# Optimization experiments

Measured on AMD Instinct MI355X. Metric: run time of the kernel, lower is better.

Reference implementation:

```python
import jax, jax.numpy as jnp
import numpy as np

WINDOW_SIZE = 7
C1 = 0.01 ** 2
C2 = 0.03 ** 2


def _gaussian_window(ws: int) -> jnp.ndarray:
    sigma = ws / 6.0
    coords = jnp.arange(ws, dtype=jnp.float32) - ws // 2
    g = jnp.exp(-coords ** 2 / (2 * sigma ** 2))
    g = g / g.sum()
    k3 = g[:, None, None] * g[None, :, None] * g[None, None, :]
    k3 = k3 / k3.sum()
    return k3.reshape(1, 1, ws, ws, ws)  # OIDHW


def _conv3d_same(x, w):
    pad = WINDOW_SIZE // 2
    return jax.lax.conv_general_dilated(
        x, w, window_strides=(1, 1, 1),
        padding=[(pad, pad)] * 3,
        dimension_numbers=('NCDHW', 'OIDHW', 'NCDHW'))


def setup_inputs() -> dict:
    key = jax.random.key(0)
    k1, k2 = jax.random.split(key)
    shape = (2, 1, 160, 160, 160)
    predicted = jax.random.uniform(k1, shape, dtype=jnp.float32)
    target = jax.random.uniform(k2, shape, dtype=jnp.float32)
    return {"predicted": predicted, "target": target}


def reference(predicted, target):
    window = _gaussian_window(WINDOW_SIZE)
    mu1 = _conv3d_same(predicted, window)
    mu2 = _conv3d_same(target, window)
    mu1_sq = mu1 ** 2
    mu2_sq = mu2 ** 2
    mu1_mu2 = mu1 * mu2
    sigma1_sq = _conv3d_same(predicted ** 2, window) - mu1_sq
    sigma2_sq = _conv3d_same(target ** 2, window) - mu2_sq
    sigma12 = _conv3d_same(predicted * target, window) - mu1_mu2
    ssim_map = ((2 * mu1_mu2 + C1) * (2 * sigma12 + C2)) / (
        (mu1_sq + mu2_sq + C1) * (sigma1_sq + sigma2_sq + C2))
    return 1.0 - ssim_map.mean()
```

## Files before the change

kernel.cpp:

```cpp
#include <hip/hip_runtime.h>
#include <math.h>

#define DD 160
#define HH 160
#define WW 160
#define NB 2
#define NEL (NB*DD*HH*WW)

#define XT 32
#define YT 16
#define ZC 16
#define NTHR 256
#define NZCH (DD/ZC)
#define GX (WW/XT)
#define GY (HH/YT)
#define NBLK (GX*GY*NB*NZCH)
#define NPART (NBLK*4)

#define HR 22
#define NJOB (HR*8)
#define CP 35

typedef float v2f __attribute__((ext_vector_type(2)));

struct G7 { float g[7]; };

__global__ __launch_bounds__(NTHR, 4) void ssim_fused(
        const float* __restrict__ p, const float* __restrict__ t,
        float* __restrict__ partial, G7 gw) {
    const int tid = threadIdx.x;
    const int lane = tid & 63, wv = tid >> 6;
    const int tx  = tid & 31;
    const int tyo = tid >> 5;

    const int flat = blockIdx.x;
    const int w = (flat & 7) * (NBLK / 8) + (flat >> 3);
    const int bx = w % GX;
    const int by = (w / GX) % GY;
    const int bz = w / (GX * GY);

    const int x0 = bx * XT;
    const int y0 = by * YT;
    const int n  = bz / NZCH;
    const int zs = (bz % NZCH) * ZC;
    const int send = zs + ZC + 3;

    __shared__ float4 c4[2][HR][CP];

    v2f r01[2][6], r23[2][6];
#pragma unroll
    for (int yo = 0; yo < 2; ++yo)
#pragma unroll
        for (int j = 0; j < 6; ++j) {
            r01[yo][j] = (v2f)(0.f);
            r23[yo][j] = (v2f)(0.f);
        }

    const float C1v = 1e-4f, C2v = 9e-4f;
    float ssum = 0.f;
    const int hw = HH * WW;
    const float* pv = p + (size_t)n * DD * hw;
    const float* tv = t + (size_t)n * DD * hw;

    const int br = tid >> 3;
    const int bxg = tid & 7;
    const int bgy = y0 + br - 3;
    const bool jok = tid < NJOB;
    const bool browok = jok && (unsigned)bgy < (unsigned)HH;
    const int cbase = x0 + 4 * bxg - 4;
    const int pcr = tx + (tx >> 3);
    bool qok[3];
#pragma unroll
    for (int q = 0; q < 3; ++q)
        qok[q] = browok && (unsigned)(cbase + 4 * q) < (unsigned)WW;

    const float* prow = pv + (size_t)(zs - 3) * hw + bgy * WW;
    const float* trow = tv + (size_t)(zs - 3) * hw + bgy * WW;

    float4 pfa[3], pfb[3];
    auto prefetch = [&](int sx) {
#pragma unroll
        for (int q = 0; q < 3; ++q) {
            pfa[q] = make_float4(0.f, 0.f, 0.f, 0.f);
            pfb[q] = make_float4(0.f, 0.f, 0.f, 0.f);
        }
        if (sx >= 0 && sx < DD && sx < send) {
#pragma unroll
            for (int q = 0; q < 3; ++q) {
                if (qok[q]) {
                    pfa[q] = *(const float4*)(prow + cbase + 4 * q);
                    pfb[q] = *(const float4*)(trow + cbase + 4 * q);
                }
            }
        }
    };

    auto do_B = [&](int par) {
        if (jok) {
            v2f s01[4], s23[4];
#pragma unroll
            for (int e = 0; e < 4; ++e) { s01[e] = (v2f)(0.f); s23[e] = (v2f)(0.f); }
#pragma unroll
            for (int q = 0; q < 3; ++q) {
                const float af[4] = {pfa[q].x, pfa[q].y, pfa[q].z, pfa[q].w};
                const float bf[4] = {pfb[q].x, pfb[q].y, pfb[q].z, pfb[q].w};
#pragma unroll
                for (int jj = 0; jj < 4; ++jj) {
                    const int i = 4 * q + jj;
                    v2f pt; pt[0] = af[jj]; pt[1] = bf[jj];
                    v2f ud; ud[0] = af[jj] + bf[jj]; ud[1] = af[jj] - bf[jj];
                    v2f qu = ud * ud;
#pragma unroll
                    for (int e = 0; e < 4; ++e) {
                        const int k = i - e - 1;
                        if (k >= 0 && k < 7) {
                            s01[e] = gw.g[k] * pt + s01[e];
                            s23[e] = gw.g[k] * qu + s23[e];
                        }
                    }
                }
            }
#pragma unroll
            for (int e = 0; e < 4; ++e) {
                int c = 4 * bxg + e;
                c4[par][br][c + (c >> 3)] =
                    make_float4(s01[e][0], s01[e][1], s23[e][0], s23[e][1]);
            }
        }
    };

    prefetch(zs - 3);
    do_B((zs - 3) & 1);
    prow += hw; trow += hw;
    prefetch(zs - 2);

    for (int s = zs - 3; s < send; ++s) {
        __syncthreads();

        const bool cvalid = (s >= 0) && (s < DD);
        float4 cv[8];
        if (cvalid) {
#pragma unroll
            for (int r8 = 0; r8 < 8; ++r8)
                cv[r8] = c4[s & 1][2 * tyo + r8][pcr];
        }
        __builtin_amdgcn_sched_barrier(0);

        if (s + 1 < send) do_B((s + 1) & 1);

        prow += hw; trow += hw;
        prefetch(s + 2);

        v2f m01[2], m23[2];
#pragma unroll
        for (int yo = 0; yo < 2; ++yo) {
            m01[yo] = (v2f)(0.f);
            m23[yo] = (v2f)(0.f);
        }
        if (cvalid) {
#pragma unroll
            for (int r8 = 0; r8 < 8; ++r8) {
                float4 v = cv[r8];
                v2f v01; v01[0] = v.x; v01[1] = v.y;
                v2f v23; v23[0] = v.z; v23[1] = v.w;
                if (r8 < 7) {
                    float w2 = gw.g[r8];
                    m01[0] = w2 * v01 + m01[0];
                    m23[0] = w2 * v23 + m23[0];
                }
                if (r8 > 0) {
                    float w2 = gw.g[r8 - 1];
                    m01[1] = w2 * v01 + m01[1];
                    m23[1] = w2 * v23 + m23[1];
                }
            }
        }

#pragma unroll
        for (int yo = 0; yo < 2; ++yo) {
            v2f v01 = m01[yo], v23 = m23[yo];
            v2f cons01 = gw.g[6] * v01 + r01[yo][0];
            v2f cons23 = gw.g[6] * v23 + r23[yo][0];
#pragma unroll
            for (int jj = 0; jj < 5; ++jj) {
                r01[yo][jj] = gw.g[5 - jj] * v01 + r01[yo][jj + 1];
                r23[yo][jj] = gw.g[5 - jj] * v23 + r23[yo][jj + 1];
            }
            r01[yo][5] = gw.g[0] * v01;
            r23[yo][5] = gw.g[0] * v23;

            if (s >= zs + 3) {
                float mu1 = cons01[0], mu2 = cons01[1];
                float Eu  = cons23[0], Ew  = cons23[1];
                float mu12 = mu1 * mu2, mu1sq = mu1 * mu1, mu2sq = mu2 * mu2;
                float sumsq = 0.5f  * (Eu + Ew) - mu1sq - mu2sq;
                float s12   = 0.25f * (Eu - Ew) - mu12;
                float num = (2.f * mu12 + C1v) * (2.f * s12 + C2v);
                float den = (mu1sq + mu2sq + C1v) * (sumsq + C2v);
                ssum += num * __builtin_amdgcn_rcpf(den);
            }
        }
    }

#pragma unroll
    for (int off = 32; off > 0; off >>= 1)
        ssum += __shfl_down(ssum, off, 64);
    if (lane == 0)
        partial[flat * 4 + wv] = ssum;
}

__global__ __launch_bounds__(256) void ssim_final(
        const float* __restrict__ partial, float* __restrict__ out) {
    float s = 0.f;
    for (int i = threadIdx.x; i < NPART; i += 256) s += partial[i];
#pragma unroll
    for (int off = 32; off > 0; off >>= 1)
        s += __shfl_down(s, off, 64);
    __shared__ float wsum[4];
    int lane = threadIdx.x & 63, wid = threadIdx.x >> 6;
    if (lane == 0) wsum[wid] = s;
    __syncthreads();
    if (threadIdx.x == 0) {
        float tot = wsum[0] + wsum[1] + wsum[2] + wsum[3];
        out[0] = 1.0f - tot / (float)NEL;
    }
}

extern "C" void kernel_launch(void* const* d_in, const int* in_sizes, int n_in,
                              void* d_out, int out_size, void* d_ws, size_t ws_size,
                              hipStream_t stream) {
    const float* p = (const float*)d_in[0];
    const float* t = (const float*)d_in[1];
    float* out = (float*)d_out;
    float* partial = (float*)d_ws;

    G7 gw;
    {
        double s = 0.0, sig = 7.0 / 6.0;
        double g[7];
        for (int i = 0; i < 7; ++i) {
            double d = (double)i - 3.0;
            g[i] = exp(-d * d / (2.0 * sig * sig));
            s += g[i];
        }
        for (int i = 0; i < 7; ++i) gw.g[i] = (float)(g[i] / s);
    }

    ssim_fused<<<NBLK, NTHR, 0, stream>>>(p, t, partial, gw);
    ssim_final<<<1, 256, 0, stream>>>(partial, out);
}
```

Measured before the change: 133.0 us.

## Give each wavefront a private LDS tile to remove block-wide barriers

```diff
diff --git a/kernel.cpp b/kernel.cpp
--- a/kernel.cpp
+++ b/kernel.cpp
@@ -17,9 +17,9 @@
 #define NBLK (GX*GY*NB*NZCH)
 #define NPART (NBLK*4)
 
+#define WX 8
 #define HR 22
-#define NJOB (HR*8)
-#define CP 35
+#define CPW 9
 
 typedef float v2f __attribute__((ext_vector_type(2)));
 
@@ -28,10 +28,9 @@
 __global__ __launch_bounds__(NTHR, 4) void ssim_fused(
         const float* __restrict__ p, const float* __restrict__ t,
         float* __restrict__ partial, G7 gw) {
-    const int tid = threadIdx.x;
-    const int lane = tid & 63, wv = tid >> 6;
-    const int tx  = tid & 31;
-    const int tyo = tid >> 5;
+    const int tid  = threadIdx.x;
+    const int lane = tid & 63;
+    const int wv   = tid >> 6;
 
     const int flat = blockIdx.x;
     const int w = (flat & 7) * (NBLK / 8) + (flat >> 3);
@@ -39,13 +38,14 @@
     const int by = (w / GX) % GY;
     const int bz = w / (GX * GY);
 
-    const int x0 = bx * XT;
-    const int y0 = by * YT;
-    const int n  = bz / NZCH;
-    const int zs = (bz % NZCH) * ZC;
+    const int x0w = bx * XT + wv * WX;
+    const int y0  = by * YT;
+    const int n   = bz / NZCH;
+    const int zs  = (bz % NZCH) * ZC;
     const int send = zs + ZC + 3;
 
-    __shared__ float4 c4[2][HR][CP];
+    __shared__ float4 c4s[4][HR][CPW];
+    float4 (*cw)[CPW] = c4s[wv];
 
     v2f r01[2][6], r23[2][6];
 #pragma unroll
@@ -62,17 +62,19 @@
     const float* pv = p + (size_t)n * DD * hw;
     const float* tv = t + (size_t)n * DD * hw;
 
-    const int br = tid >> 3;
-    const int bxg = tid & 7;
-    const int bgy = y0 + br - 3;
-    const bool jok = tid < NJOB;
+    const bool jok = lane < 2 * HR;
+    const int brow = lane >> 1;
+    const int grp  = lane & 1;
+    const int bgy  = y0 + brow - 3;
     const bool browok = jok && (unsigned)bgy < (unsigned)HH;
-    const int cbase = x0 + 4 * bxg - 4;
-    const int pcr = tx + (tx >> 3);
+    const int cbase = x0w + 4 * grp - 4;
     bool qok[3];
 #pragma unroll
     for (int q = 0; q < 3; ++q)
         qok[q] = browok && (unsigned)(cbase + 4 * q) < (unsigned)WW;
+
+    const int cx = lane & 7;
+    const int yg = lane >> 3;
 
     const float* prow = pv + (size_t)(zs - 3) * hw + bgy * WW;
     const float* trow = tv + (size_t)(zs - 3) * hw + bgy * WW;
@@ -95,61 +97,10 @@
         }
     };
 
-    auto do_B = [&](int par) {
-        if (jok) {
-            v2f s01[4], s23[4];
-#pragma unroll
-            for (int e = 0; e < 4; ++e) { s01[e] = (v2f)(0.f); s23[e] = (v2f)(0.f); }
-#pragma unroll
-            for (int q = 0; q < 3; ++q) {
-                const float af[4] = {pfa[q].x, pfa[q].y, pfa[q].z, pfa[q].w};
-                const float bf[4] = {pfb[q].x, pfb[q].y, pfb[q].z, pfb[q].w};
-#pragma unroll
-                for (int jj = 0; jj < 4; ++jj) {
-                    const int i = 4 * q + jj;
-                    v2f pt; pt[0] = af[jj]; pt[1] = bf[jj];
-                    v2f ud; ud[0] = af[jj] + bf[jj]; ud[1] = af[jj] - bf[jj];
-                    v2f qu = ud * ud;
-#pragma unroll
-                    for (int e = 0; e < 4; ++e) {
-                        const int k = i - e - 1;
-                        if (k >= 0 && k < 7) {
-                            s01[e] = gw.g[k] * pt + s01[e];
-                            s23[e] = gw.g[k] * qu + s23[e];
-                        }
-                    }
-                }
-            }
-#pragma unroll
-            for (int e = 0; e < 4; ++e) {
-                int c = 4 * bxg + e;
-                c4[par][br][c + (c >> 3)] =
-                    make_float4(s01[e][0], s01[e][1], s23[e][0], s23[e][1]);
-            }
-        }
-    };
-
     prefetch(zs - 3);
-    do_B((zs - 3) & 1);
-    prow += hw; trow += hw;
-    prefetch(zs - 2);
 
     for (int s = zs - 3; s < send; ++s) {
-        __syncthreads();
-
-        const bool cvalid = (s >= 0) && (s < DD);
-        float4 cv[8];
-        if (cvalid) {
-#pragma unroll
-            for (int r8 = 0; r8 < 8; ++r8)
-                cv[r8] = c4[s & 1][2 * tyo + r8][pcr];
-        }
-        __builtin_amdgcn_sched_barrier(0);
-
-        if (s + 1 < send) do_B((s + 1) & 1);
-
-        prow += hw; trow += hw;
-        prefetch(s + 2);
+        const bool valid = (s >= 0) && (s < DD);
 
         v2f m01[2], m23[2];
 #pragma unroll
@@ -157,10 +108,44 @@
             m01[yo] = (v2f)(0.f);
             m23[yo] = (v2f)(0.f);
         }
-        if (cvalid) {
+
+        if (valid) {
+            if (jok) {
+                v2f s01[4], s23[4];
+#pragma unroll
+                for (int e = 0; e < 4; ++e) { s01[e] = (v2f)(0.f); s23[e] = (v2f)(0.f); }
+#pragma unroll
+                for (int q = 0; q < 3; ++q) {
+                    const float af[4] = {pfa[q].x, pfa[q].y, pfa[q].z, pfa[q].w};
+                    const float bf[4] = {pfb[q].x, pfb[q].y, pfb[q].z, pfb[q].w};
+#pragma unroll
+                    for (int jj = 0; jj < 4; ++jj) {
+                        const int i = 4 * q + jj;
+                        v2f pt; pt[0] = af[jj]; pt[1] = bf[jj];
+                        v2f ud; ud[0] = af[jj] + bf[jj]; ud[1] = af[jj] - bf[jj];
+                        v2f qu = ud * ud;
+#pragma unroll
+                        for (int e = 0; e < 4; ++e) {
+                            const int k = i - e - 1;
+                            if (k >= 0 && k < 7) {
+                                s01[e] = gw.g[k] * pt + s01[e];
+                                s23[e] = gw.g[k] * qu + s23[e];
+                            }
+                        }
+                    }
+                }
+#pragma unroll
+                for (int e = 0; e < 4; ++e)
+                    cw[brow][4 * grp + e] =
+                        make_float4(s01[e][0], s01[e][1], s23[e][0], s23[e][1]);
+            }
+
+            prow += hw; trow += hw;
+            prefetch(s + 1);
+
 #pragma unroll
             for (int r8 = 0; r8 < 8; ++r8) {
-                float4 v = cv[r8];
+                float4 v = cw[2 * yg + r8][cx];
                 v2f v01; v01[0] = v.x; v01[1] = v.y;
                 v2f v23; v23[0] = v.z; v23[1] = v.w;
                 if (r8 < 7) {
@@ -174,6 +159,9 @@
                     m23[1] = w2 * v23 + m23[1];
                 }
             }
+        } else {
+            prow += hw; trow += hw;
+            prefetch(s + 1);
         }
 
 #pragma unroll
```

New measurement: 131.4 us. Within noise of the previous version (-1.2%).
